# Performance work log

Hardware: AMD Instinct MI355X
Metric: run time of the kernel (lower is better)

The kernel has to match this reference:

```python
import jax, jax.numpy as jnp
import numpy as np

B, N, C, H = 8, 2048, 384, 6
D = C // H  # head dim = 64
SCALE = D ** -0.5


def setup_inputs() -> dict:
    key = jax.random.key(0)
    k1, k2, k3, k4 = jax.random.split(key, 4)
    x = jax.random.normal(k1, (B, N, C), dtype=jnp.float32)
    prompt = jnp.zeros((1,), dtype=jnp.float32)  # unused by forward
    mask = jax.random.uniform(k2, (B, N, N), dtype=jnp.float32)
    qkv_w = jax.random.normal(k3, (3 * C, C), dtype=jnp.float32) * (C ** -0.5)
    proj_w = jax.random.normal(k4, (C, C), dtype=jnp.float32) * (C ** -0.5)
    proj_b = jnp.zeros((C,), dtype=jnp.float32)
    return {"x": x, "prompt": prompt, "mask": mask,
            "qkv_w": qkv_w, "proj_w": proj_w, "proj_b": proj_b}


def reference(x, prompt, mask, qkv_w, proj_w, proj_b):
    b, n, c = x.shape
    # qkv: Linear(dim, 3*dim, bias=False) -> (B,N,3,H,D) -> (3,B,H,N,D)
    qkv = (x @ qkv_w.T).reshape(b, n, 3, H, D).transpose(2, 0, 3, 1, 4)
    q, k, v = qkv[0], qkv[1], qkv[2]
    # attn scores with additive mask (mask * -1e5), softmax over keys
    attn = jnp.einsum('bhqd,bhkd->bhqk', q, k) * SCALE
    attn = attn + (mask * -100000.0)[:, None, :, :]
    attn = jax.nn.softmax(attn, axis=-1)
    out = jnp.einsum('bhqk,bhkd->bhqd', attn, v)  # (B,H,N,D)
    out = out.transpose(0, 2, 1, 3).reshape(b, n, c)
    return out @ proj_w.T + proj_b
```

## Files before the change

kernel.cpp:

```cpp
#include <hip/hip_runtime.h>
#include <stdint.h>
#include <math.h>

#define BB 8
#define SEQ 2048
#define CDIM 384
#define NH 6
#define HD 64
#define QKVN 1152

typedef __attribute__((ext_vector_type(8))) __bf16 bf16x8;
typedef __attribute__((ext_vector_type(4))) float f32x4;
typedef __attribute__((ext_vector_type(4))) unsigned short ushort4v;

__device__ __forceinline__ unsigned short f2bf(float f) {
  unsigned int u = __float_as_uint(f);
  u += 0x7fffu + ((u >> 16) & 1u);
  return (unsigned short)(u >> 16);
}

__global__ void k_convert(const float* __restrict__ src, unsigned short* __restrict__ dst, int n4) {
  int i = blockIdx.x * blockDim.x + threadIdx.x;
  if (i >= n4) return;
  float4 f = reinterpret_cast<const float4*>(src)[i];
  ushort4v u;
  u.x = f2bf(f.x); u.y = f2bf(f.y); u.z = f2bf(f.z); u.w = f2bf(f.w);
  reinterpret_cast<ushort4v*>(dst)[i] = u;
}

__device__ __forceinline__ void gload_lds16(const unsigned short* g, unsigned short* l) {
  __builtin_amdgcn_global_load_lds((const __attribute__((address_space(1))) void*)g,
                                   (__attribute__((address_space(3))) void*)l, 16, 0, 0);
}

template<int OUT_F32>
__global__ __launch_bounds__(256, 2) void k_gemm_bt(
    const unsigned short* __restrict__ A, const unsigned short* __restrict__ Bm,
    unsigned short* __restrict__ Cb, float* __restrict__ Cf,
    const float* __restrict__ bias, int M, int Nc, int K)
{
  __shared__ unsigned short lA[128 * 32];
  __shared__ unsigned short lB[128 * 32];
  const int t = threadIdx.x;
  const int w = t >> 6, l = t & 63;
  const int wr = w >> 1, wc = w & 1;
  const int row0 = blockIdx.x * 128, col0 = blockIdx.y * 128;
  const f32x4 vzero = {0.f, 0.f, 0.f, 0.f};
  f32x4 acc[4][4];
#pragma unroll
  for (int m = 0; m < 4; ++m)
#pragma unroll
    for (int n = 0; n < 4; ++n) acc[m][n] = vzero;

  const int srow = w * 16 + (l >> 2);
  const int scol = (l & 3) * 8;
  const int lr = l & 15, kc = (l >> 4) * 8;

  for (int k0 = 0; k0 < K; k0 += 32) {
#pragma unroll
    for (int r = 0; r < 2; ++r) {
      gload_lds16(A + (size_t)(row0 + r * 64 + srow) * K + k0 + scol,
                  &lA[(r * 64 + srow) * 32 + scol]);
      gload_lds16(Bm + (size_t)(col0 + r * 64 + srow) * K + k0 + scol,
                  &lB[(r * 64 + srow) * 32 + scol]);
    }
    __syncthreads();
    bf16x8 af[4], bfr[4];
#pragma unroll
    for (int m = 0; m < 4; ++m)
      af[m] = *(const bf16x8*)&lA[(wr * 64 + m * 16 + lr) * 32 + kc];
#pragma unroll
    for (int n = 0; n < 4; ++n)
      bfr[n] = *(const bf16x8*)&lB[(wc * 64 + n * 16 + lr) * 32 + kc];
#pragma unroll
    for (int m = 0; m < 4; ++m)
#pragma unroll
      for (int n = 0; n < 4; ++n)
        acc[m][n] = __builtin_amdgcn_mfma_f32_16x16x32_bf16(af[m], bfr[n], acc[m][n], 0, 0, 0);
    __syncthreads();
  }

#pragma unroll
  for (int m = 0; m < 4; ++m) {
    const int row = row0 + wr * 64 + m * 16 + (l >> 4) * 4;
#pragma unroll
    for (int n = 0; n < 4; ++n) {
      const int col = col0 + wc * 64 + n * 16 + (l & 15);
      if (OUT_F32) {
        const float bv = bias[col];
#pragma unroll
        for (int j = 0; j < 4; ++j)
          Cf[(size_t)(row + j) * Nc + col] = acc[m][n][j] + bv;
      } else {
#pragma unroll
        for (int j = 0; j < 4; ++j)
          Cb[(size_t)(row + j) * Nc + col] = f2bf(acc[m][n][j]);
      }
    }
  }
}

__global__ void k_vtrans(const unsigned short* __restrict__ qkv, unsigned short* __restrict__ vt)
{
  __shared__ unsigned short tile[64][76];
  const int bh = blockIdx.x;
  const int b = bh / NH, h = bh - b * NH;
  const int n0 = blockIdx.y * 64;
  const int t = threadIdx.x;
  const int rr0 = t >> 4;
  const int c4 = (t & 15) * 4;
  const unsigned short* src = qkv + (size_t)(b * SEQ + n0) * QKVN + 2 * CDIM + h * HD;
#pragma unroll
  for (int rr = 0; rr < 4; ++rr) {
    int n = rr * 16 + rr0;
    ushort4v v = *(const ushort4v*)(src + (size_t)n * QKVN + c4);
    *(ushort4v*)&tile[n][c4] = v;
  }
  __syncthreads();
  unsigned short* dst = vt + (size_t)bh * HD * SEQ + n0;
#pragma unroll
  for (int rr = 0; rr < 4; ++rr) {
    int d = rr * 16 + rr0;
    ushort4v v;
    v.x = tile[c4 + 0][d];
    v.y = tile[c4 + 1][d];
    v.z = tile[c4 + 2][d];
    v.w = tile[c4 + 3][d];
    *(ushort4v*)(dst + (size_t)d * SEQ + c4) = v;
  }
}

__global__ __launch_bounds__(256, 4) void k_attn(
    const unsigned short* __restrict__ qkv, const float* __restrict__ mask,
    const unsigned short* __restrict__ vt, unsigned short* __restrict__ aout)
{
  const int bid = blockIdx.x;
  const int b = bid & 7;
  const int g2 = bid >> 3;
  const int h = g2 % NH;
  const int nt = g2 / NH;
  const int t = threadIdx.x;
  const int w = t >> 6, l = t & 63;
  const int gk = l >> 4, c = l & 15;
  const int q0 = nt * 64 + w * 16;

  __shared__ unsigned short lK[2][4096];
  __shared__ unsigned short lV[2][4096];
  __shared__ unsigned int lP[4][512];
  unsigned int* prow = lP[w] + c * 32;

  const unsigned short* qb = qkv + (size_t)(b * SEQ + q0) * QKVN + h * HD;
  const unsigned short* kb = qkv + (size_t)(b * SEQ) * QKVN + CDIM + h * HD;
  const unsigned short* vb = vt + (size_t)(b * NH + h) * HD * SEQ;
  const float* mrowc = mask + ((size_t)b * SEQ + q0 + c) * SEQ;

  const int trow = t >> 3, tg = t & 7;
  const int glog = tg ^ (trow & 7);
  const size_t kSrc = (size_t)trow * QKVN + glog * 8;
  const size_t vSrc = (size_t)trow * SEQ + glog * 8;

  const int fr0 = c * 64 + ((gk) ^ (c & 7)) * 8;
  const int fr1 = c * 64 + ((4 + gk) ^ (c & 7)) * 8;
  const int cx = (c & 7) << 2;

  bf16x8 qf0 = *(const bf16x8*)(qb + (size_t)c * QKVN + gk * 8);
  bf16x8 qf1 = *(const bf16x8*)(qb + (size_t)c * QKVN + 32 + gk * 8);
#pragma unroll
  for (int i = 0; i < 8; ++i) {
    qf0[i] = (__bf16)((float)qf0[i] * 0.18033688f);
    qf1[i] = (__bf16)((float)qf1[i] * 0.18033688f);
  }

  const f32x4 vzero = {0.f, 0.f, 0.f, 0.f};
  f32x4 acco[4];
  float mreg = -INFINITY, asum = 0.f;
#pragma unroll
  for (int dt = 0; dt < 4; ++dt) acco[dt] = vzero;

#pragma unroll
  for (int j = 0; j < 2; ++j) {
    gload_lds16(kb + (size_t)j * 32 * QKVN + kSrc, &lK[0][j * 2048 + t * 8]);
    gload_lds16(vb + (size_t)j * 32 * SEQ + vSrc, &lV[0][j * 2048 + t * 8]);
  }
  float4 mk[4];
#pragma unroll
  for (int j = 0; j < 4; ++j)
    mk[j] = *(const float4*)(mrowc + 16 * j + 4 * gk);
  int buf = 0;

  for (int kt = 0; kt < SEQ; kt += 64) {
    const bool haveNext = (kt + 64 < SEQ);
    __syncthreads();
    if (haveNext) {
#pragma unroll
      for (int j = 0; j < 2; ++j) {
        gload_lds16(kb + (size_t)(kt + 64 + j * 32) * QKVN + kSrc, &lK[buf ^ 1][j * 2048 + t * 8]);
        gload_lds16(vb + (kt + 64) + (size_t)j * 32 * SEQ + vSrc, &lV[buf ^ 1][j * 2048 + t * 8]);
      }
    }

    f32x4 s[4];
#pragma unroll
    for (int j = 0; j < 4; ++j) {
      bf16x8 kfa = *(const bf16x8*)&lK[buf][j * 1024 + fr0];
      bf16x8 kfb = *(const bf16x8*)&lK[buf][j * 1024 + fr1];
      s[j] = __builtin_amdgcn_mfma_f32_16x16x32_bf16(kfa, qf0, vzero, 0, 0, 0);
      s[j] = __builtin_amdgcn_mfma_f32_16x16x32_bf16(kfb, qf1, s[j], 0, 0, 0);
    }

#pragma unroll
    for (int j = 0; j < 4; ++j) {
      const float* mkf = (const float*)&mk[j];
#pragma unroll
      for (int r = 0; r < 4; ++r)
        s[j][r] = fmaf(mkf[r], -144269.50f, s[j][r]);
    }

    if (haveNext) {
#pragma unroll
      for (int j = 0; j < 4; ++j)
        mk[j] = *(const float4*)(mrowc + kt + 64 + 16 * j + 4 * gk);
    }

    float tm = fmaxf(fmaxf(fmaxf(s[0][0], s[0][1]), fmaxf(s[0][2], s[0][3])),
                     fmaxf(fmaxf(s[1][0], s[1][1]), fmaxf(s[1][2], s[1][3])));
    tm = fmaxf(tm, fmaxf(fmaxf(fmaxf(s[2][0], s[2][1]), fmaxf(s[2][2], s[2][3])),
                         fmaxf(fmaxf(s[3][0], s[3][1]), fmaxf(s[3][2], s[3][3]))));
    tm = fmaxf(tm, __shfl_xor(tm, 16));
    tm = fmaxf(tm, __shfl_xor(tm, 32));

    if (__any(tm > mreg + 8.f)) {
      const float mn = fmaxf(mreg, tm);
      const float al = __builtin_amdgcn_exp2f(mreg - mn);
      mreg = mn;
      asum *= al;
      float alr[4];
#pragma unroll
      for (int r = 0; r < 4; ++r)
        alr[r] = __shfl(al, 20 * gk + r);
#pragma unroll
      for (int dt = 0; dt < 4; ++dt)
#pragma unroll
        for (int r = 0; r < 4; ++r)
          acco[dt][r] *= alr[r];
    }

#pragma unroll
    for (int j = 0; j < 4; ++j)
#pragma unroll
      for (int r = 0; r < 4; ++r)
        s[j][r] = __builtin_amdgcn_exp2f(s[j][r] - mreg);
    float rs = ((s[0][0] + s[0][1]) + (s[0][2] + s[0][3]))
             + ((s[1][0] + s[1][1]) + (s[1][2] + s[1][3]))
             + ((s[2][0] + s[2][1]) + (s[2][2] + s[2][3]))
             + ((s[3][0] + s[3][1]) + (s[3][2] + s[3][3]));
    rs += __shfl_xor(rs, 16);
    rs += __shfl_xor(rs, 32);
    asum += rs;

    unsigned int pk[8];
#pragma unroll
    for (int j = 0; j < 4; ++j) {
      asm("v_cvt_pk_bf16_f32 %0, %1, %2" : "=v"(pk[2 * j]) : "v"(s[j][0]), "v"(s[j][1]));
      asm("v_cvt_pk_bf16_f32 %0, %1, %2" : "=v"(pk[2 * j + 1]) : "v"(s[j][2]), "v"(s[j][3]));
    }
    __asm__ volatile("" ::: "memory");
#pragma unroll
    for (int j = 0; j < 4; ++j) {
      prow[(8 * j + 2 * gk + 0) ^ cx] = pk[2 * j];
      prow[(8 * j + 2 * gk + 1) ^ cx] = pk[2 * j + 1];
    }
    __asm__ volatile("" ::: "memory");
    bf16x8 pf0 = *(const bf16x8*)(prow + ((4 * gk) ^ cx));
    bf16x8 pf1 = *(const bf16x8*)(prow + ((16 + 4 * gk) ^ cx));
    __asm__ volatile("" ::: "memory");

#pragma unroll
    for (int dt = 0; dt < 4; ++dt) {
      bf16x8 vf0 = *(const bf16x8*)&lV[buf][dt * 1024 + fr0];
      bf16x8 vf1 = *(const bf16x8*)&lV[buf][dt * 1024 + fr1];
      acco[dt] = __builtin_amdgcn_mfma_f32_16x16x32_bf16(pf0, vf0, acco[dt], 0, 0, 0);
      acco[dt] = __builtin_amdgcn_mfma_f32_16x16x32_bf16(pf1, vf1, acco[dt], 0, 0, 0);
    }
    buf ^= 1;
  }

  float invr[4];
#pragma unroll
  for (int r = 0; r < 4; ++r)
    invr[r] = 1.0f / __shfl(asum, 20 * gk + r);
  unsigned short* ob = aout + (size_t)(b * SEQ + q0) * CDIM + h * HD;
#pragma unroll
  for (int r = 0; r < 4; ++r)
#pragma unroll
    for (int dt = 0; dt < 4; ++dt)
      ob[(size_t)(4 * gk + r) * CDIM + dt * 16 + c] = f2bf(acco[dt][r] * invr[r]);
}

extern "C" void kernel_launch(void* const* d_in, const int* in_sizes, int n_in,
                              void* d_out, int out_size, void* d_ws, size_t ws_size,
                              hipStream_t stream) {
  (void)in_sizes; (void)n_in; (void)out_size; (void)ws_size;
  const float* x      = (const float*)d_in[0];
  const float* mask   = (const float*)d_in[2];
  const float* qkv_w  = (const float*)d_in[3];
  const float* proj_w = (const float*)d_in[4];
  const float* proj_b = (const float*)d_in[5];
  float* out = (float*)d_out;
  char* ws = (char*)d_ws;

  unsigned short* xb    = (unsigned short*)(ws + 0);
  unsigned short* wqb   = (unsigned short*)(ws + 12582912);
  unsigned short* wpb   = (unsigned short*)(ws + 13467648);
  unsigned short* qkvb  = (unsigned short*)(ws + 13762560);
  unsigned short* vtb   = (unsigned short*)(ws + 51511296);
  unsigned short* aoutb = (unsigned short*)(ws + 64094208);

  k_convert<<<6144, 256, 0, stream>>>(x, xb, 1572864);
  k_convert<<<432, 256, 0, stream>>>(qkv_w, wqb, 110592);
  k_convert<<<144, 256, 0, stream>>>(proj_w, wpb, 36864);
  k_gemm_bt<0><<<dim3(128, 9), 256, 0, stream>>>(xb, wqb, qkvb, nullptr, nullptr, 16384, 1152, 384);
  k_vtrans<<<dim3(48, 32), 256, 0, stream>>>(qkvb, vtb);
  k_attn<<<1536, 256, 0, stream>>>(qkvb, mask, vtb, aoutb);
  k_gemm_bt<1><<<dim3(128, 3), 256, 0, stream>>>(aoutb, wpb, nullptr, out, proj_b, 16384, 384, 384);
}
```

Before: 191.1 us.

## Process two query tiles per wave in attention to reuse K/V loads

```diff
diff --git a/kernel.cpp b/kernel.cpp
--- a/kernel.cpp
+++ b/kernel.cpp
@@ -12,6 +12,7 @@
 typedef __attribute__((ext_vector_type(8))) __bf16 bf16x8;
 typedef __attribute__((ext_vector_type(4))) float f32x4;
 typedef __attribute__((ext_vector_type(4))) unsigned short ushort4v;
+typedef __attribute__((ext_vector_type(2))) unsigned int uint2v;
 
 __device__ __forceinline__ unsigned short f2bf(float f) {
   unsigned int u = __float_as_uint(f);
@@ -142,17 +143,20 @@
   const int t = threadIdx.x;
   const int w = t >> 6, l = t & 63;
   const int gk = l >> 4, c = l & 15;
-  const int q0 = nt * 64 + w * 16;
+  const int q0 = nt * 128 + w * 16;
 
   __shared__ unsigned short lK[2][4096];
   __shared__ unsigned short lV[2][4096];
-  __shared__ unsigned int lP[4][512];
-  unsigned int* prow = lP[w] + c * 32;
-
-  const unsigned short* qb = qkv + (size_t)(b * SEQ + q0) * QKVN + h * HD;
+  __shared__ unsigned int lP[4][2][512];
+  unsigned int* prow0 = &lP[w][0][c * 32];
+  unsigned int* prow1 = &lP[w][1][c * 32];
+
+  const unsigned short* qb0 = qkv + (size_t)(b * SEQ + q0) * QKVN + h * HD;
+  const unsigned short* qb1 = qb0 + (size_t)64 * QKVN;
   const unsigned short* kb = qkv + (size_t)(b * SEQ) * QKVN + CDIM + h * HD;
   const unsigned short* vb = vt + (size_t)(b * NH + h) * HD * SEQ;
-  const float* mrowc = mask + ((size_t)b * SEQ + q0 + c) * SEQ;
+  const float* mrow0 = mask + ((size_t)b * SEQ + q0 + c) * SEQ + 4 * gk;
+  const float* mrow1 = mrow0 + (size_t)64 * SEQ;
 
   const int trow = t >> 3, tg = t & 7;
   const int glog = tg ^ (trow & 7);
@@ -163,29 +167,29 @@
   const int fr1 = c * 64 + ((4 + gk) ^ (c & 7)) * 8;
   const int cx = (c & 7) << 2;
 
-  bf16x8 qf0 = *(const bf16x8*)(qb + (size_t)c * QKVN + gk * 8);
-  bf16x8 qf1 = *(const bf16x8*)(qb + (size_t)c * QKVN + 32 + gk * 8);
+  bf16x8 qf00 = *(const bf16x8*)(qb0 + (size_t)c * QKVN + gk * 8);
+  bf16x8 qf01 = *(const bf16x8*)(qb0 + (size_t)c * QKVN + 32 + gk * 8);
+  bf16x8 qf10 = *(const bf16x8*)(qb1 + (size_t)c * QKVN + gk * 8);
+  bf16x8 qf11 = *(const bf16x8*)(qb1 + (size_t)c * QKVN + 32 + gk * 8);
 #pragma unroll
   for (int i = 0; i < 8; ++i) {
-    qf0[i] = (__bf16)((float)qf0[i] * 0.18033688f);
-    qf1[i] = (__bf16)((float)qf1[i] * 0.18033688f);
+    qf00[i] = (__bf16)((float)qf00[i] * 0.18033688f);
+    qf01[i] = (__bf16)((float)qf01[i] * 0.18033688f);
+    qf10[i] = (__bf16)((float)qf10[i] * 0.18033688f);
+    qf11[i] = (__bf16)((float)qf11[i] * 0.18033688f);
   }
 
   const f32x4 vzero = {0.f, 0.f, 0.f, 0.f};
-  f32x4 acco[4];
-  float mreg = -INFINITY, asum = 0.f;
-#pragma unroll
-  for (int dt = 0; dt < 4; ++dt) acco[dt] = vzero;
+  f32x4 acco0[4], acco1[4];
+  float mreg0 = -INFINITY, asum0 = 0.f, mreg1 = -INFINITY, asum1 = 0.f;
+#pragma unroll
+  for (int dt = 0; dt < 4; ++dt) { acco0[dt] = vzero; acco1[dt] = vzero; }
 
 #pragma unroll
   for (int j = 0; j < 2; ++j) {
     gload_lds16(kb + (size_t)j * 32 * QKVN + kSrc, &lK[0][j * 2048 + t * 8]);
     gload_lds16(vb + (size_t)j * 32 * SEQ + vSrc, &lV[0][j * 2048 + t * 8]);
   }
-  float4 mk[4];
-#pragma unroll
-  for (int j = 0; j < 4; ++j)
-    mk[j] = *(const float4*)(mrowc + 16 * j + 4 * gk);
   int buf = 0;
 
   for (int kt = 0; kt < SEQ; kt += 64) {
@@ -199,102 +203,142 @@
       }
     }
 
-    f32x4 s[4];
+    float4 mk0[4], mk1[4];
+#pragma unroll
+    for (int j = 0; j < 4; ++j) {
+      mk0[j] = *(const float4*)(mrow0 + kt + 16 * j);
+      mk1[j] = *(const float4*)(mrow1 + kt + 16 * j);
+    }
+
+    f32x4 s0[4], s1[4];
 #pragma unroll
     for (int j = 0; j < 4; ++j) {
       bf16x8 kfa = *(const bf16x8*)&lK[buf][j * 1024 + fr0];
       bf16x8 kfb = *(const bf16x8*)&lK[buf][j * 1024 + fr1];
-      s[j] = __builtin_amdgcn_mfma_f32_16x16x32_bf16(kfa, qf0, vzero, 0, 0, 0);
-      s[j] = __builtin_amdgcn_mfma_f32_16x16x32_bf16(kfb, qf1, s[j], 0, 0, 0);
+      s0[j] = __builtin_amdgcn_mfma_f32_16x16x32_bf16(kfa, qf00, vzero, 0, 0, 0);
+      s0[j] = __builtin_amdgcn_mfma_f32_16x16x32_bf16(kfb, qf01, s0[j], 0, 0, 0);
+      s1[j] = __builtin_amdgcn_mfma_f32_16x16x32_bf16(kfa, qf10, vzero, 0, 0, 0);
+      s1[j] = __builtin_amdgcn_mfma_f32_16x16x32_bf16(kfb, qf11, s1[j], 0, 0, 0);
     }
 
 #pragma unroll
     for (int j = 0; j < 4; ++j) {
-      const float* mkf = (const float*)&mk[j];
-#pragma unroll
-      for (int r = 0; r < 4; ++r)
-        s[j][r] = fmaf(mkf[r], -144269.50f, s[j][r]);
-    }
-
-    if (haveNext) {
-#pragma unroll
-      for (int j = 0; j < 4; ++j)
-        mk[j] = *(const float4*)(mrowc + kt + 64 + 16 * j + 4 * gk);
-    }
-
-    float tm = fmaxf(fmaxf(fmaxf(s[0][0], s[0][1]), fmaxf(s[0][2], s[0][3])),
-                     fmaxf(fmaxf(s[1][0], s[1][1]), fmaxf(s[1][2], s[1][3])));
-    tm = fmaxf(tm, fmaxf(fmaxf(fmaxf(s[2][0], s[2][1]), fmaxf(s[2][2], s[2][3])),
-                         fmaxf(fmaxf(s[3][0], s[3][1]), fmaxf(s[3][2], s[3][3]))));
-    tm = fmaxf(tm, __shfl_xor(tm, 16));
-    tm = fmaxf(tm, __shfl_xor(tm, 32));
-
-    if (__any(tm > mreg + 8.f)) {
-      const float mn = fmaxf(mreg, tm);
-      const float al = __builtin_amdgcn_exp2f(mreg - mn);
-      mreg = mn;
-      asum *= al;
+      const float* m0 = (const float*)&mk0[j];
+      const float* m1 = (const float*)&mk1[j];
+#pragma unroll
+      for (int r = 0; r < 4; ++r) {
+        s0[j][r] = fmaf(m0[r], -144269.50f, s0[j][r]);
+        s1[j][r] = fmaf(m1[r], -144269.50f, s1[j][r]);
+      }
+    }
+
+    float tm0 = fmaxf(fmaxf(fmaxf(s0[0][0], s0[0][1]), fmaxf(s0[0][2], s0[0][3])),
+                      fmaxf(fmaxf(s0[1][0], s0[1][1]), fmaxf(s0[1][2], s0[1][3])));
+    tm0 = fmaxf(tm0, fmaxf(fmaxf(fmaxf(s0[2][0], s0[2][1]), fmaxf(s0[2][2], s0[2][3])),
+                           fmaxf(fmaxf(s0[3][0], s0[3][1]), fmaxf(s0[3][2], s0[3][3]))));
+    float tm1 = fmaxf(fmaxf(fmaxf(s1[0][0], s1[0][1]), fmaxf(s1[0][2], s1[0][3])),
+                      fmaxf(fmaxf(s1[1][0], s1[1][1]), fmaxf(s1[1][2], s1[1][3])));
+    tm1 = fmaxf(tm1, fmaxf(fmaxf(fmaxf(s1[2][0], s1[2][1]), fmaxf(s1[2][2], s1[2][3])),
+                           fmaxf(fmaxf(s1[3][0], s1[3][1]), fmaxf(s1[3][2], s1[3][3]))));
+    tm0 = fmaxf(tm0, __shfl_xor(tm0, 16));
+    tm0 = fmaxf(tm0, __shfl_xor(tm0, 32));
+    tm1 = fmaxf(tm1, __shfl_xor(tm1, 16));
+    tm1 = fmaxf(tm1, __shfl_xor(tm1, 32));
+
+    if (__any(tm0 > mreg0 + 8.f)) {
+      const float mn = fmaxf(mreg0, tm0);
+      const float al = __builtin_amdgcn_exp2f(mreg0 - mn);
+      mreg0 = mn;
+      asum0 *= al;
       float alr[4];
 #pragma unroll
-      for (int r = 0; r < 4; ++r)
-        alr[r] = __shfl(al, 20 * gk + r);
+      for (int r = 0; r < 4; ++r) alr[r] = __shfl(al, 20 * gk + r);
 #pragma unroll
       for (int dt = 0; dt < 4; ++dt)
 #pragma unroll
-        for (int r = 0; r < 4; ++r)
-          acco[dt][r] *= alr[r];
+        for (int r = 0; r < 4; ++r) acco0[dt][r] *= alr[r];
+    }
+    if (__any(tm1 > mreg1 + 8.f)) {
+      const float mn = fmaxf(mreg1, tm1);
+      const float al = __builtin_amdgcn_exp2f(mreg1 - mn);
+      mreg1 = mn;
+      asum1 *= al;
+      float alr[4];
+#pragma unroll
+      for (int r = 0; r < 4; ++r) alr[r] = __shfl(al, 20 * gk + r);
+#pragma unroll
+      for (int dt = 0; dt < 4; ++dt)
+#pragma unroll
+        for (int r = 0; r < 4; ++r) acco1[dt][r] *= alr[r];
     }
 
 #pragma unroll
     for (int j = 0; j < 4; ++j)
 #pragma unroll
-      for (int r = 0; r < 4; ++r)
-        s[j][r] = __builtin_amdgcn_exp2f(s[j][r] - mreg);
-    float rs = ((s[0][0] + s[0][1]) + (s[0][2] + s[0][3]))
-             + ((s[1][0] + s[1][1]) + (s[1][2] + s[1][3]))
-             + ((s[2][0] + s[2][1]) + (s[2][2] + s[2][3]))
-             + ((s[3][0] + s[3][1]) + (s[3][2] + s[3][3]));
-    rs += __shfl_xor(rs, 16);
-    rs += __shfl_xor(rs, 32);
-    asum += rs;
-
-    unsigned int pk[8];
+      for (int r = 0; r < 4; ++r) {
+        s0[j][r] = __builtin_amdgcn_exp2f(s0[j][r] - mreg0);
+        s1[j][r] = __builtin_amdgcn_exp2f(s1[j][r] - mreg1);
+      }
+    float rs0 = ((s0[0][0] + s0[0][1]) + (s0[0][2] + s0[0][3]))
+              + ((s0[1][0] + s0[1][1]) + (s0[1][2] + s0[1][3]))
+              + ((s0[2][0] + s0[2][1]) + (s0[2][2] + s0[2][3]))
+              + ((s0[3][0] + s0[3][1]) + (s0[3][2] + s0[3][3]));
+    float rs1 = ((s1[0][0] + s1[0][1]) + (s1[0][2] + s1[0][3]))
+              + ((s1[1][0] + s1[1][1]) + (s1[1][2] + s1[1][3]))
+              + ((s1[2][0] + s1[2][1]) + (s1[2][2] + s1[2][3]))
+              + ((s1[3][0] + s1[3][1]) + (s1[3][2] + s1[3][3]));
+    rs0 += __shfl_xor(rs0, 16);
+    rs0 += __shfl_xor(rs0, 32);
+    rs1 += __shfl_xor(rs1, 16);
+    rs1 += __shfl_xor(rs1, 32);
+    asum0 += rs0;
+    asum1 += rs1;
+
+    __asm__ volatile("" ::: "memory");
 #pragma unroll
     for (int j = 0; j < 4; ++j) {
-      asm("v_cvt_pk_bf16_f32 %0, %1, %2" : "=v"(pk[2 * j]) : "v"(s[j][0]), "v"(s[j][1]));
-      asm("v_cvt_pk_bf16_f32 %0, %1, %2" : "=v"(pk[2 * j + 1]) : "v"(s[j][2]), "v"(s[j][3]));
+      uint2v pr0, pr1;
+      asm("v_cvt_pk_bf16_f32 %0, %1, %2" : "=v"(pr0.x) : "v"(s0[j][0]), "v"(s0[j][1]));
+      asm("v_cvt_pk_bf16_f32 %0, %1, %2" : "=v"(pr0.y) : "v"(s0[j][2]), "v"(s0[j][3]));
+      asm("v_cvt_pk_bf16_f32 %0, %1, %2" : "=v"(pr1.x) : "v"(s1[j][0]), "v"(s1[j][1]));
+      asm("v_cvt_pk_bf16_f32 %0, %1, %2" : "=v"(pr1.y) : "v"(s1[j][2]), "v"(s1[j][3]));
+      *(uint2v*)(prow0 + ((8 * j + 2 * gk) ^ cx)) = pr0;
+      *(uint2v*)(prow1 + ((8 * j + 2 * gk) ^ cx)) = pr1;
     }
     __asm__ volatile("" ::: "memory");
-#pragma unroll
-    for (int j = 0; j < 4; ++j) {
-      prow[(8 * j + 2 * gk + 0) ^ cx] = pk[2 * j];
-      prow[(8 * j + 2 * gk + 1) ^ cx] = pk[2 * j + 1];
-    }
-    __asm__ volatile("" ::: "memory");
-    bf16x8 pf0 = *(const bf16x8*)(prow + ((4 * gk) ^ cx));
-    bf16x8 pf1 = *(const bf16x8*)(prow + ((16 + 4 * gk) ^ cx));
+    bf16x8 pf00 = *(const bf16x8*)(prow0 + ((4 * gk) ^ cx));
+    bf16x8 pf01 = *(const bf16x8*)(prow0 + ((16 + 4 * gk) ^ cx));
+    bf16x8 pf10 = *(const bf16x8*)(prow1 + ((4 * gk) ^ cx));
+    bf16x8 pf11 = *(const bf16x8*)(prow1 + ((16 + 4 * gk) ^ cx));
     __asm__ volatile("" ::: "memory");
 
 #pragma unroll
     for (int dt = 0; dt < 4; ++dt) {
       bf16x8 vf0 = *(const bf16x8*)&lV[buf][dt * 1024 + fr0];
       bf16x8 vf1 = *(const bf16x8*)&lV[buf][dt * 1024 + fr1];
-      acco[dt] = __builtin_amdgcn_mfma_f32_16x16x32_bf16(pf0, vf0, acco[dt], 0, 0, 0);
-      acco[dt] = __builtin_amdgcn_mfma_f32_16x16x32_bf16(pf1, vf1, acco[dt], 0, 0, 0);
+      acco0[dt] = __builtin_amdgcn_mfma_f32_16x16x32_bf16(pf00, vf0, acco0[dt], 0, 0, 0);
+      acco0[dt] = __builtin_amdgcn_mfma_f32_16x16x32_bf16(pf01, vf1, acco0[dt], 0, 0, 0);
+      acco1[dt] = __builtin_amdgcn_mfma_f32_16x16x32_bf16(pf10, vf0, acco1[dt], 0, 0, 0);
+      acco1[dt] = __builtin_amdgcn_mfma_f32_16x16x32_bf16(pf11, vf1, acco1[dt], 0, 0, 0);
     }
     buf ^= 1;
   }
 
-  float invr[4];
+  float inv0[4], inv1[4];
+#pragma unroll
+  for (int r = 0; r < 4; ++r) {
+    inv0[r] = 1.0f / __shfl(asum0, 20 * gk + r);
+    inv1[r] = 1.0f / __shfl(asum1, 20 * gk + r);
+  }
+  unsigned short* ob0 = aout + (size_t)(b * SEQ + q0) * CDIM + h * HD;
+  unsigned short* ob1 = ob0 + (size_t)64 * CDIM;
 #pragma unroll
   for (int r = 0; r < 4; ++r)
-    invr[r] = 1.0f / __shfl(asum, 20 * gk + r);
-  unsigned short* ob = aout + (size_t)(b * SEQ + q0) * CDIM + h * HD;
-#pragma unroll
-  for (int r = 0; r < 4; ++r)
-#pragma unroll
-    for (int dt = 0; dt < 4; ++dt)
-      ob[(size_t)(4 * gk + r) * CDIM + dt * 16 + c] = f2bf(acco[dt][r] * invr[r]);
+#pragma unroll
+    for (int dt = 0; dt < 4; ++dt) {
+      ob0[(size_t)(4 * gk + r) * CDIM + dt * 16 + c] = f2bf(acco0[dt][r] * inv0[r]);
+      ob1[(size_t)(4 * gk + r) * CDIM + dt * 16 + c] = f2bf(acco1[dt][r] * inv1[r]);
+    }
 }
 
 extern "C" void kernel_launch(void* const* d_in, const int* in_sizes, int n_in,
@@ -321,6 +365,6 @@
   k_convert<<<144, 256, 0, stream>>>(proj_w, wpb, 36864);
   k_gemm_bt<0><<<dim3(128, 9), 256, 0, stream>>>(xb, wqb, qkvb, nullptr, nullptr, 16384, 1152, 384);
   k_vtrans<<<dim3(48, 32), 256, 0, stream>>>(qkvb, vtb);
-  k_attn<<<1536, 256, 0, stream>>>(qkvb, mask, vtb, aoutb);
+  k_attn<<<768, 256, 0, stream>>>(qkvb, mask, vtb, aoutb);
   k_gemm_bt<1><<<dim3(128, 3), 256, 0, stream>>>(aoutb, wpb, nullptr, out, proj_b, 16384, 384, 384);
 }
```

Measured after the change: 241.9 us. 26.6% more time.

## Replace double-buffered LDS DMA with register-staged single-buffer K/V prefetch

Applied to the files above, without the earlier changes.

```diff
diff --git a/kernel.cpp b/kernel.cpp
--- a/kernel.cpp
+++ b/kernel.cpp
@@ -12,6 +12,8 @@
 typedef __attribute__((ext_vector_type(8))) __bf16 bf16x8;
 typedef __attribute__((ext_vector_type(4))) float f32x4;
 typedef __attribute__((ext_vector_type(4))) unsigned short ushort4v;
+typedef __attribute__((ext_vector_type(8))) unsigned short ushort8v;
+typedef __attribute__((ext_vector_type(2))) unsigned int uint2v;
 
 __device__ __forceinline__ unsigned short f2bf(float f) {
   unsigned int u = __float_as_uint(f);
@@ -130,7 +132,7 @@
   }
 }
 
-__global__ __launch_bounds__(256, 4) void k_attn(
+__global__ __launch_bounds__(256, 6) void k_attn(
     const unsigned short* __restrict__ qkv, const float* __restrict__ mask,
     const unsigned short* __restrict__ vt, unsigned short* __restrict__ aout)
 {
@@ -144,20 +146,20 @@
   const int gk = l >> 4, c = l & 15;
   const int q0 = nt * 64 + w * 16;
 
-  __shared__ unsigned short lK[2][4096];
-  __shared__ unsigned short lV[2][4096];
+  __shared__ unsigned short lK[4096];
+  __shared__ unsigned short lV[4096];
   __shared__ unsigned int lP[4][512];
   unsigned int* prow = lP[w] + c * 32;
 
   const unsigned short* qb = qkv + (size_t)(b * SEQ + q0) * QKVN + h * HD;
   const unsigned short* kb = qkv + (size_t)(b * SEQ) * QKVN + CDIM + h * HD;
   const unsigned short* vb = vt + (size_t)(b * NH + h) * HD * SEQ;
-  const float* mrowc = mask + ((size_t)b * SEQ + q0 + c) * SEQ;
+  const float* mrowc = mask + ((size_t)b * SEQ + q0 + c) * SEQ + 4 * gk;
 
   const int trow = t >> 3, tg = t & 7;
-  const int glog = tg ^ (trow & 7);
-  const size_t kSrc = (size_t)trow * QKVN + glog * 8;
-  const size_t vSrc = (size_t)trow * SEQ + glog * 8;
+  const size_t kSrc = (size_t)trow * QKVN + tg * 8;
+  const size_t vSrc = (size_t)trow * SEQ + tg * 8;
+  const int ldst = trow * 64 + (tg ^ (trow & 7)) * 8;
 
   const int fr0 = c * 64 + ((gk) ^ (c & 7)) * 8;
   const int fr1 = c * 64 + ((4 + gk) ^ (c & 7)) * 8;
@@ -177,37 +179,52 @@
 #pragma unroll
   for (int dt = 0; dt < 4; ++dt) acco[dt] = vzero;
 
-#pragma unroll
-  for (int j = 0; j < 2; ++j) {
-    gload_lds16(kb + (size_t)j * 32 * QKVN + kSrc, &lK[0][j * 2048 + t * 8]);
-    gload_lds16(vb + (size_t)j * 32 * SEQ + vSrc, &lV[0][j * 2048 + t * 8]);
+  {
+    ushort8v k0 = *(const ushort8v*)(kb + kSrc);
+    ushort8v k1 = *(const ushort8v*)(kb + (size_t)32 * QKVN + kSrc);
+    ushort8v v0 = *(const ushort8v*)(vb + vSrc);
+    ushort8v v1 = *(const ushort8v*)(vb + (size_t)32 * SEQ + vSrc);
+    *(ushort8v*)&lK[ldst] = k0;
+    *(ushort8v*)&lK[2048 + ldst] = k1;
+    *(ushort8v*)&lV[ldst] = v0;
+    *(ushort8v*)&lV[2048 + ldst] = v1;
   }
   float4 mk[4];
 #pragma unroll
   for (int j = 0; j < 4; ++j)
-    mk[j] = *(const float4*)(mrowc + 16 * j + 4 * gk);
-  int buf = 0;
+    mk[j] = *(const float4*)(mrowc + 16 * j);
+  __syncthreads();
 
   for (int kt = 0; kt < SEQ; kt += 64) {
     const bool haveNext = (kt + 64 < SEQ);
-    __syncthreads();
-    if (haveNext) {
-#pragma unroll
-      for (int j = 0; j < 2; ++j) {
-        gload_lds16(kb + (size_t)(kt + 64 + j * 32) * QKVN + kSrc, &lK[buf ^ 1][j * 2048 + t * 8]);
-        gload_lds16(vb + (kt + 64) + (size_t)j * 32 * SEQ + vSrc, &lV[buf ^ 1][j * 2048 + t * 8]);
-      }
+
+    ushort8v kr0, kr1;
+    if (haveNext) {
+      kr0 = *(const ushort8v*)(kb + (size_t)(kt + 64) * QKVN + kSrc);
+      kr1 = *(const ushort8v*)(kb + (size_t)(kt + 96) * QKVN + kSrc);
     }
 
     f32x4 s[4];
 #pragma unroll
     for (int j = 0; j < 4; ++j) {
-      bf16x8 kfa = *(const bf16x8*)&lK[buf][j * 1024 + fr0];
-      bf16x8 kfb = *(const bf16x8*)&lK[buf][j * 1024 + fr1];
+      bf16x8 kfa = *(const bf16x8*)&lK[j * 1024 + fr0];
+      bf16x8 kfb = *(const bf16x8*)&lK[j * 1024 + fr1];
       s[j] = __builtin_amdgcn_mfma_f32_16x16x32_bf16(kfa, qf0, vzero, 0, 0, 0);
       s[j] = __builtin_amdgcn_mfma_f32_16x16x32_bf16(kfb, qf1, s[j], 0, 0, 0);
     }
 
+    __syncthreads();
+    if (haveNext) {
+      *(ushort8v*)&lK[ldst] = kr0;
+      *(ushort8v*)&lK[2048 + ldst] = kr1;
+    }
+
+    ushort8v vr0, vr1;
+    if (haveNext) {
+      vr0 = *(const ushort8v*)(vb + (kt + 64) + vSrc);
+      vr1 = *(const ushort8v*)(vb + (kt + 64) + (size_t)32 * SEQ + vSrc);
+    }
+
 #pragma unroll
     for (int j = 0; j < 4; ++j) {
       const float* mkf = (const float*)&mk[j];
@@ -219,7 +236,7 @@
     if (haveNext) {
 #pragma unroll
       for (int j = 0; j < 4; ++j)
-        mk[j] = *(const float4*)(mrowc + kt + 64 + 16 * j + 4 * gk);
+        mk[j] = *(const float4*)(mrowc + kt + 64 + 16 * j);
     }
 
     float tm = fmaxf(fmaxf(fmaxf(s[0][0], s[0][1]), fmaxf(s[0][2], s[0][3])),
@@ -258,17 +275,13 @@
     rs += __shfl_xor(rs, 32);
     asum += rs;
 
-    unsigned int pk[8];
+    __asm__ volatile("" ::: "memory");
 #pragma unroll
     for (int j = 0; j < 4; ++j) {
-      asm("v_cvt_pk_bf16_f32 %0, %1, %2" : "=v"(pk[2 * j]) : "v"(s[j][0]), "v"(s[j][1]));
-      asm("v_cvt_pk_bf16_f32 %0, %1, %2" : "=v"(pk[2 * j + 1]) : "v"(s[j][2]), "v"(s[j][3]));
-    }
-    __asm__ volatile("" ::: "memory");
-#pragma unroll
-    for (int j = 0; j < 4; ++j) {
-      prow[(8 * j + 2 * gk + 0) ^ cx] = pk[2 * j];
-      prow[(8 * j + 2 * gk + 1) ^ cx] = pk[2 * j + 1];
+      uint2v pr;
+      asm("v_cvt_pk_bf16_f32 %0, %1, %2" : "=v"(pr.x) : "v"(s[j][0]), "v"(s[j][1]));
+      asm("v_cvt_pk_bf16_f32 %0, %1, %2" : "=v"(pr.y) : "v"(s[j][2]), "v"(s[j][3]));
+      *(uint2v*)(prow + ((8 * j + 2 * gk) ^ cx)) = pr;
     }
     __asm__ volatile("" ::: "memory");
     bf16x8 pf0 = *(const bf16x8*)(prow + ((4 * gk) ^ cx));
@@ -277,12 +290,17 @@
 
 #pragma unroll
     for (int dt = 0; dt < 4; ++dt) {
-      bf16x8 vf0 = *(const bf16x8*)&lV[buf][dt * 1024 + fr0];
-      bf16x8 vf1 = *(const bf16x8*)&lV[buf][dt * 1024 + fr1];
+      bf16x8 vf0 = *(const bf16x8*)&lV[dt * 1024 + fr0];
+      bf16x8 vf1 = *(const bf16x8*)&lV[dt * 1024 + fr1];
       acco[dt] = __builtin_amdgcn_mfma_f32_16x16x32_bf16(pf0, vf0, acco[dt], 0, 0, 0);
       acco[dt] = __builtin_amdgcn_mfma_f32_16x16x32_bf16(pf1, vf1, acco[dt], 0, 0, 0);
     }
-    buf ^= 1;
+
+    __syncthreads();
+    if (haveNext) {
+      *(ushort8v*)&lV[ldst] = vr0;
+      *(ushort8v*)&lV[2048 + ldst] = vr1;
+    }
   }
 
   float invr[4];
```

After: 554.7 us. 2.9x slower.

## Load K/V MFMA fragments directly from global memory instead of LDS staging

Applied to the files above, without the earlier changes.

```diff
diff --git a/kernel.cpp b/kernel.cpp
--- a/kernel.cpp
+++ b/kernel.cpp
@@ -12,6 +12,7 @@
 typedef __attribute__((ext_vector_type(8))) __bf16 bf16x8;
 typedef __attribute__((ext_vector_type(4))) float f32x4;
 typedef __attribute__((ext_vector_type(4))) unsigned short ushort4v;
+typedef __attribute__((ext_vector_type(2))) unsigned int uint2v;
 
 __device__ __forceinline__ unsigned short f2bf(float f) {
   unsigned int u = __float_as_uint(f);
@@ -130,7 +131,7 @@
   }
 }
 
-__global__ __launch_bounds__(256, 4) void k_attn(
+__global__ __launch_bounds__(256, 5) void k_attn(
     const unsigned short* __restrict__ qkv, const float* __restrict__ mask,
     const unsigned short* __restrict__ vt, unsigned short* __restrict__ aout)
 {
@@ -144,24 +145,16 @@
   const int gk = l >> 4, c = l & 15;
   const int q0 = nt * 64 + w * 16;
 
-  __shared__ unsigned short lK[2][4096];
-  __shared__ unsigned short lV[2][4096];
   __shared__ unsigned int lP[4][512];
   unsigned int* prow = lP[w] + c * 32;
+  const int cx = (c & 7) << 2;
 
   const unsigned short* qb = qkv + (size_t)(b * SEQ + q0) * QKVN + h * HD;
-  const unsigned short* kb = qkv + (size_t)(b * SEQ) * QKVN + CDIM + h * HD;
-  const unsigned short* vb = vt + (size_t)(b * NH + h) * HD * SEQ;
-  const float* mrowc = mask + ((size_t)b * SEQ + q0 + c) * SEQ;
-
-  const int trow = t >> 3, tg = t & 7;
-  const int glog = tg ^ (trow & 7);
-  const size_t kSrc = (size_t)trow * QKVN + glog * 8;
-  const size_t vSrc = (size_t)trow * SEQ + glog * 8;
-
-  const int fr0 = c * 64 + ((gk) ^ (c & 7)) * 8;
-  const int fr1 = c * 64 + ((4 + gk) ^ (c & 7)) * 8;
-  const int cx = (c & 7) << 2;
+  const unsigned short* kbase = qkv + (size_t)(b * SEQ) * QKVN + CDIM + h * HD
+                                + (size_t)c * QKVN + gk * 8;
+  const unsigned short* vbase = vt + (size_t)(b * NH + h) * HD * SEQ
+                                + (size_t)c * SEQ + gk * 8;
+  const float* mrowc = mask + ((size_t)b * SEQ + q0 + c) * SEQ + 4 * gk;
 
   bf16x8 qf0 = *(const bf16x8*)(qb + (size_t)c * QKVN + gk * 8);
   bf16x8 qf1 = *(const bf16x8*)(qb + (size_t)c * QKVN + 32 + gk * 8);
@@ -177,35 +170,34 @@
 #pragma unroll
   for (int dt = 0; dt < 4; ++dt) acco[dt] = vzero;
 
-#pragma unroll
-  for (int j = 0; j < 2; ++j) {
-    gload_lds16(kb + (size_t)j * 32 * QKVN + kSrc, &lK[0][j * 2048 + t * 8]);
-    gload_lds16(vb + (size_t)j * 32 * SEQ + vSrc, &lV[0][j * 2048 + t * 8]);
-  }
   float4 mk[4];
 #pragma unroll
   for (int j = 0; j < 4; ++j)
-    mk[j] = *(const float4*)(mrowc + 16 * j + 4 * gk);
-  int buf = 0;
+    mk[j] = *(const float4*)(mrowc + 16 * j);
 
   for (int kt = 0; kt < SEQ; kt += 64) {
     const bool haveNext = (kt + 64 < SEQ);
-    __syncthreads();
-    if (haveNext) {
-#pragma unroll
-      for (int j = 0; j < 2; ++j) {
-        gload_lds16(kb + (size_t)(kt + 64 + j * 32) * QKVN + kSrc, &lK[buf ^ 1][j * 2048 + t * 8]);
-        gload_lds16(vb + (kt + 64) + (size_t)j * 32 * SEQ + vSrc, &lV[buf ^ 1][j * 2048 + t * 8]);
-      }
-    }
-
+
+    bf16x8 kf[4][2];
+#pragma unroll
+    for (int j = 0; j < 4; ++j) {
+      const unsigned short* kr = kbase + (size_t)(kt + 16 * j) * QKVN;
+      kf[j][0] = *(const bf16x8*)(kr);
+      kf[j][1] = *(const bf16x8*)(kr + 32);
+    }
     f32x4 s[4];
 #pragma unroll
     for (int j = 0; j < 4; ++j) {
-      bf16x8 kfa = *(const bf16x8*)&lK[buf][j * 1024 + fr0];
-      bf16x8 kfb = *(const bf16x8*)&lK[buf][j * 1024 + fr1];
-      s[j] = __builtin_amdgcn_mfma_f32_16x16x32_bf16(kfa, qf0, vzero, 0, 0, 0);
-      s[j] = __builtin_amdgcn_mfma_f32_16x16x32_bf16(kfb, qf1, s[j], 0, 0, 0);
+      s[j] = __builtin_amdgcn_mfma_f32_16x16x32_bf16(kf[j][0], qf0, vzero, 0, 0, 0);
+      s[j] = __builtin_amdgcn_mfma_f32_16x16x32_bf16(kf[j][1], qf1, s[j], 0, 0, 0);
+    }
+
+    bf16x8 vf[4][2];
+#pragma unroll
+    for (int dt = 0; dt < 4; ++dt) {
+      const unsigned short* vr = vbase + (size_t)(dt * 16) * SEQ + kt;
+      vf[dt][0] = *(const bf16x8*)(vr);
+      vf[dt][1] = *(const bf16x8*)(vr + 32);
     }
 
 #pragma unroll
@@ -219,7 +211,7 @@
     if (haveNext) {
 #pragma unroll
       for (int j = 0; j < 4; ++j)
-        mk[j] = *(const float4*)(mrowc + kt + 64 + 16 * j + 4 * gk);
+        mk[j] = *(const float4*)(mrowc + kt + 64 + 16 * j);
     }
 
     float tm = fmaxf(fmaxf(fmaxf(s[0][0], s[0][1]), fmaxf(s[0][2], s[0][3])),
@@ -258,17 +250,13 @@
     rs += __shfl_xor(rs, 32);
     asum += rs;
 
-    unsigned int pk[8];
+    __asm__ volatile("" ::: "memory");
 #pragma unroll
     for (int j = 0; j < 4; ++j) {
-      asm("v_cvt_pk_bf16_f32 %0, %1, %2" : "=v"(pk[2 * j]) : "v"(s[j][0]), "v"(s[j][1]));
-      asm("v_cvt_pk_bf16_f32 %0, %1, %2" : "=v"(pk[2 * j + 1]) : "v"(s[j][2]), "v"(s[j][3]));
-    }
-    __asm__ volatile("" ::: "memory");
-#pragma unroll
-    for (int j = 0; j < 4; ++j) {
-      prow[(8 * j + 2 * gk + 0) ^ cx] = pk[2 * j];
-      prow[(8 * j + 2 * gk + 1) ^ cx] = pk[2 * j + 1];
+      uint2v pr;
+      asm("v_cvt_pk_bf16_f32 %0, %1, %2" : "=v"(pr.x) : "v"(s[j][0]), "v"(s[j][1]));
+      asm("v_cvt_pk_bf16_f32 %0, %1, %2" : "=v"(pr.y) : "v"(s[j][2]), "v"(s[j][3]));
+      *(uint2v*)(prow + ((8 * j + 2 * gk) ^ cx)) = pr;
     }
     __asm__ volatile("" ::: "memory");
     bf16x8 pf0 = *(const bf16x8*)(prow + ((4 * gk) ^ cx));
@@ -277,12 +265,9 @@
 
 #pragma unroll
     for (int dt = 0; dt < 4; ++dt) {
-      bf16x8 vf0 = *(const bf16x8*)&lV[buf][dt * 1024 + fr0];
-      bf16x8 vf1 = *(const bf16x8*)&lV[buf][dt * 1024 + fr1];
-      acco[dt] = __builtin_amdgcn_mfma_f32_16x16x32_bf16(pf0, vf0, acco[dt], 0, 0, 0);
-      acco[dt] = __builtin_amdgcn_mfma_f32_16x16x32_bf16(pf1, vf1, acco[dt], 0, 0, 0);
-    }
-    buf ^= 1;
+      acco[dt] = __builtin_amdgcn_mfma_f32_16x16x32_bf16(pf0, vf[dt][0], acco[dt], 0, 0, 0);
+      acco[dt] = __builtin_amdgcn_mfma_f32_16x16x32_bf16(pf1, vf[dt][1], acco[dt], 0, 0, 0);
+    }
   }
 
   float invr[4];
```

Result: slower. 584.0 us (+205.6%).
